# Kernel optimization log

Hardware: AMD Instinct MI355X
Metric: run time of the kernel (lower is better)

The kernel has to match this reference:

```python
import jax, jax.numpy as jnp
import numpy as np


def setup_inputs() -> dict:
    B, I, H = 4096, 512, 1024
    key = jax.random.key(0)
    ks = jax.random.split(key, 10)
    return {
        "input": jax.random.normal(ks[0], (B, I), dtype=jnp.float32),
        "t": jax.random.uniform(ks[1], (B, 1), dtype=jnp.float32),
        "hx": jax.random.normal(ks[2], (B, H), dtype=jnp.float32),
        "cx": jax.random.normal(ks[3], (B, H), dtype=jnp.float32),
        "weight_ih": jax.random.normal(ks[4], (4 * H, I), dtype=jnp.float32),
        "weight_hh": jax.random.normal(ks[5], (4 * H, H), dtype=jnp.float32),
        "bias_ih": jax.random.normal(ks[6], (4 * H,), dtype=jnp.float32),
        "bias_hh": jax.random.normal(ks[7], (4 * H,), dtype=jnp.float32),
        "W_decomp": jax.random.normal(ks[8], (H, H), dtype=jnp.float32),
        "b_decomp": jax.random.normal(ks[9], (H,), dtype=jnp.float32),
    }


def reference(input, t, hx, cx, weight_ih, weight_hh, bias_ih, bias_hh, W_decomp, b_decomp):
    H = W_decomp.shape[0]
    # gates: [B, 4H]
    gates = input @ weight_ih.T + bias_ih + hx @ weight_hh.T + bias_hh
    ingate, forgetgate, cellgate, outgate = jnp.split(gates, 4, axis=1)
    # time-decay factor g(t): elementwise 1/t where t != 0, broadcast [B,1] -> [B,H]
    T = jnp.where(t != 0, 1.0 / jnp.where(t != 0, t, 1.0), 0.0)  # [B, 1]
    T = jnp.broadcast_to(T, (t.shape[0], H))
    # T-LSTM cell-state decomposition
    C_ST = jnp.tanh(cx @ W_decomp + b_decomp)
    cx_adj = cx - C_ST + T * C_ST
    ingate = jax.nn.sigmoid(ingate)
    forgetgate = jax.nn.sigmoid(forgetgate)
    cellgate = jnp.tanh(cellgate)
    outgate = jax.nn.sigmoid(outgate)
    cy = forgetgate * cx_adj + ingate * cellgate
    hy = outgate * jnp.tanh(cy)
    return (hy, cy)
```

## Files before the change

kernel.cpp:

```cpp
#include <hip/hip_runtime.h>
#include <cstdint>


typedef __attribute__((ext_vector_type(8))) __bf16 bf16x8;
typedef __attribute__((ext_vector_type(4))) float f32x4;

__device__ __forceinline__ unsigned short f2bf_rn(float f) {
  unsigned int u = __float_as_uint(f);
  unsigned int r = u + 0x7fffu + ((u >> 16) & 1u);
  return (unsigned short)(r >> 16);
}
__device__ __forceinline__ float bf2f(unsigned short h) {
  return __uint_as_float(((unsigned int)h) << 16);
}
__device__ __forceinline__ float sigm_f(float x) {
  return 1.0f / (1.0f + __expf(-x));
}
__device__ __forceinline__ float tanh_f(float x) {
  return 1.0f - 2.0f / (__expf(2.0f * x) + 1.0f);
}
__device__ __forceinline__ void gl_lds16(const void* g, void* l) {
  __builtin_amdgcn_global_load_lds(
      (const __attribute__((address_space(1))) void*)g,
      (__attribute__((address_space(3))) void*)l, 16, 0, 0);
}

__global__ __launch_bounds__(384) void prep_k(
    const float* __restrict__ input, const float* __restrict__ hx,
    const float* __restrict__ w_ih, const float* __restrict__ w_hh,
    const float* __restrict__ cx,
    unsigned short* __restrict__ Xhi, unsigned short* __restrict__ Xlo,
    unsigned short* __restrict__ Whi, unsigned short* __restrict__ Wlo,
    unsigned short* __restrict__ Chi, unsigned short* __restrict__ Clo) {
  const int bid = blockIdx.x;
  const int k = threadIdx.x << 2;
  const float* src;
  unsigned short *hi, *lo;
  if (bid < 4096) {
    const long m = bid;
    src = (k < 512) ? (input + m * 512 + k) : (hx + m * 1024 + (k - 512));
    hi = Xhi + m * 1536 + k;
    lo = Xlo + m * 1536 + k;
  } else if (bid < 8192) {
    const int n = bid - 4096;
    const int g = n >> 10;
    const int h = n & 1023;
    const long nd = ((h >> 5) << 7) | (g << 5) | (h & 31);
    src = (k < 512) ? (w_ih + (long)n * 512 + k) : (w_hh + (long)n * 1024 + (k - 512));
    hi = Whi + nd * 1536 + k;
    lo = Wlo + nd * 1536 + k;
  } else {
    if (k >= 1024) return;
    const long m = bid - 8192;
    src = cx + m * 1024 + k;
    hi = Chi + m * 1024 + k;
    lo = Clo + m * 1024 + k;
  }
  float4 v = *(const float4*)src;
  ushort4 hv, lv;
  hv.x = f2bf_rn(v.x); lv.x = f2bf_rn(v.x - bf2f(hv.x));
  hv.y = f2bf_rn(v.y); lv.y = f2bf_rn(v.y - bf2f(hv.y));
  hv.z = f2bf_rn(v.z); lv.z = f2bf_rn(v.z - bf2f(hv.z));
  hv.w = f2bf_rn(v.w); lv.w = f2bf_rn(v.w - bf2f(hv.w));
  *(ushort4*)hi = hv;
  *(ushort4*)lo = lv;
}

__global__ void transpose_split_k(const float* __restrict__ W, int Ndim,
                                  unsigned short* __restrict__ Thi,
                                  unsigned short* __restrict__ Tlo) {
  __shared__ float tile[64][65];
  const int bx = blockIdx.x * 64;
  const int by = blockIdx.y * 64;
  const int tx = threadIdx.x;
  for (int r = threadIdx.y; r < 64; r += 4)
    tile[r][tx] = W[(long)(by + r) * Ndim + bx + tx];
  __syncthreads();
  for (int r = threadIdx.y; r < 64; r += 4) {
    float v = tile[tx][r];
    unsigned short h = f2bf_rn(v);
    long o = (long)(bx + r) * Ndim + by + tx;
    Thi[o] = h;
    Tlo[o] = f2bf_rn(v - bf2f(h));
  }
}

__global__ __launch_bounds__(256) void gemm_mega(
    const unsigned short* __restrict__ Xh, const unsigned short* __restrict__ Xl,
    const unsigned short* __restrict__ Wh, const unsigned short* __restrict__ Wl,
    const unsigned short* __restrict__ Ch, const unsigned short* __restrict__ Cl,
    const unsigned short* __restrict__ Dh, const unsigned short* __restrict__ Dl,
    const float* __restrict__ b_ih, const float* __restrict__ b_hh,
    const float* __restrict__ b_d, const float* __restrict__ cx,
    const float* __restrict__ t, float* __restrict__ out) {
  __shared__ __align__(16) unsigned short sAh[128 * 32];
  __shared__ __align__(16) unsigned short sAl[128 * 32];
  __shared__ __align__(16) unsigned short sBh[128 * 32];
  __shared__ __align__(16) unsigned short sBl[128 * 32];

  const int n_blk = blockIdx.x & 31;
  const int m_blk = blockIdx.x >> 5;
  const int m0 = m_blk * 128;
  const int n0 = n_blk * 128;
  const int h0 = n_blk * 32;

  const int tid = threadIdx.x;
  const int wave = tid >> 6;
  const int lane = tid & 63;
  const int srow = lane >> 2;
  const int ssw = (((lane & 3) ^ ((lane >> 3) & 3)) << 3);
  const int fm = lane & 15;
  const int fq = lane >> 4;
  const int psw = (fq ^ ((fm >> 1) & 3)) << 3;

  f32x4 dacc[2][2];
#pragma unroll
  for (int i = 0; i < 2; ++i)
#pragma unroll
    for (int j = 0; j < 2; ++j) dacc[i][j] = {0.f, 0.f, 0.f, 0.f};

  {
    const unsigned short* dsrc = (wave < 2) ? Dh : Dl;
    unsigned short* ddst = ((wave < 2) ? sBh : sBl) + ((wave & 1) * 16) * 32;
    const long dgbase = (long)(h0 + (wave & 1) * 16 + srow) * 1024 + ssw;
    for (int kt = 0; kt < 1024; kt += 32) {
#pragma unroll
      for (int r = 0; r < 2; ++r) {
        const int rowb = r * 64 + wave * 16;
        const long gA = (long)(m0 + rowb + srow) * 1024 + kt + ssw;
        gl_lds16(Ch + gA, sAh + rowb * 32);
        gl_lds16(Cl + gA, sAl + rowb * 32);
      }
      gl_lds16(dsrc + dgbase + kt, ddst);
      __syncthreads();
      bf16x8 ah[2], al[2], bh[2], bl[2];
#pragma unroll
      for (int i = 0; i < 2; ++i) {
        const int ao = (wave * 32 + i * 16 + fm) * 32 + psw;
        ah[i] = *(const bf16x8*)(sAh + ao);
        al[i] = *(const bf16x8*)(sAl + ao);
        const int bo = (i * 16 + fm) * 32 + psw;
        bh[i] = *(const bf16x8*)(sBh + bo);
        bl[i] = *(const bf16x8*)(sBl + bo);
      }
#pragma unroll
      for (int i = 0; i < 2; ++i)
#pragma unroll
        for (int j = 0; j < 2; ++j) {
          dacc[i][j] = __builtin_amdgcn_mfma_f32_16x16x32_bf16(ah[i], bh[j], dacc[i][j], 0, 0, 0);
          dacc[i][j] = __builtin_amdgcn_mfma_f32_16x16x32_bf16(ah[i], bl[j], dacc[i][j], 0, 0, 0);
          dacc[i][j] = __builtin_amdgcn_mfma_f32_16x16x32_bf16(al[i], bh[j], dacc[i][j], 0, 0, 0);
        }
      __syncthreads();
    }
  }

  f32x4 acc[2][8];
#pragma unroll
  for (int i = 0; i < 2; ++i)
#pragma unroll
    for (int j = 0; j < 8; ++j) acc[i][j] = {0.f, 0.f, 0.f, 0.f};

  for (int kt = 0; kt < 1536; kt += 32) {
#pragma unroll
    for (int r = 0; r < 2; ++r) {
      const int rowb = r * 64 + wave * 16;
      const long gA = (long)(m0 + rowb + srow) * 1536 + kt + ssw;
      const long gB = (long)(n0 + rowb + srow) * 1536 + kt + ssw;
      gl_lds16(Xh + gA, sAh + rowb * 32);
      gl_lds16(Xl + gA, sAl + rowb * 32);
      gl_lds16(Wh + gB, sBh + rowb * 32);
      gl_lds16(Wl + gB, sBl + rowb * 32);
    }
    __syncthreads();
    bf16x8 ah[2], al[2];
#pragma unroll
    for (int i = 0; i < 2; ++i) {
      const int ao = (wave * 32 + i * 16 + fm) * 32 + psw;
      ah[i] = *(const bf16x8*)(sAh + ao);
      al[i] = *(const bf16x8*)(sAl + ao);
    }
#pragma unroll
    for (int jh = 0; jh < 2; ++jh) {
      bf16x8 bh[4], bl[4];
#pragma unroll
      for (int jj = 0; jj < 4; ++jj) {
        const int bo = ((jh * 4 + jj) * 16 + fm) * 32 + psw;
        bh[jj] = *(const bf16x8*)(sBh + bo);
        bl[jj] = *(const bf16x8*)(sBl + bo);
      }
#pragma unroll
      for (int i = 0; i < 2; ++i)
#pragma unroll
        for (int jj = 0; jj < 4; ++jj) {
          const int j = jh * 4 + jj;
          acc[i][j] = __builtin_amdgcn_mfma_f32_16x16x32_bf16(ah[i], bh[jj], acc[i][j], 0, 0, 0);
          acc[i][j] = __builtin_amdgcn_mfma_f32_16x16x32_bf16(ah[i], bl[jj], acc[i][j], 0, 0, 0);
          acc[i][j] = __builtin_amdgcn_mfma_f32_16x16x32_bf16(al[i], bh[jj], acc[i][j], 0, 0, 0);
        }
    }
    __syncthreads();
  }

#pragma unroll
  for (int j0 = 0; j0 < 2; ++j0) {
    const int h = h0 + j0 * 16 + fm;
    const float bsum_i = b_ih[h]           + b_hh[h];
    const float bsum_f = b_ih[1024 + h]    + b_hh[1024 + h];
    const float bsum_g = b_ih[2048 + h]    + b_hh[2048 + h];
    const float bsum_o = b_ih[3072 + h]    + b_hh[3072 + h];
    const float bd = b_d[h];
#pragma unroll
    for (int i = 0; i < 2; ++i) {
#pragma unroll
      for (int r = 0; r < 4; ++r) {
        const int m = m0 + wave * 32 + i * 16 + fq * 4 + r;
        const float tv = t[m];
        const float T = (tv != 0.0f) ? (1.0f / tv) : 0.0f;
        const float cst = tanh_f(dacc[i][j0][r] + bd);
        const float cadj = cx[(long)m * 1024 + h] + (T - 1.0f) * cst;
        const float ig = sigm_f(acc[i][0 + j0][r] + bsum_i);
        const float fg = sigm_f(acc[i][2 + j0][r] + bsum_f);
        const float cg = tanh_f(acc[i][4 + j0][r] + bsum_g);
        const float og = sigm_f(acc[i][6 + j0][r] + bsum_o);
        const float cy = fg * cadj + ig * cg;
        const float hy = og * tanh_f(cy);
        out[(long)m * 1024 + h] = hy;
        out[4096L * 1024 + (long)m * 1024 + h] = cy;
      }
    }
  }
}

extern "C" void kernel_launch(void* const* d_in, const int* in_sizes, int n_in,
                              void* d_out, int out_size, void* d_ws, size_t ws_size,
                              hipStream_t stream) {
  const float* input = (const float*)d_in[0];
  const float* t     = (const float*)d_in[1];
  const float* hx    = (const float*)d_in[2];
  const float* cx    = (const float*)d_in[3];
  const float* w_ih  = (const float*)d_in[4];
  const float* w_hh  = (const float*)d_in[5];
  const float* b_ih  = (const float*)d_in[6];
  const float* b_hh  = (const float*)d_in[7];
  const float* Wd    = (const float*)d_in[8];
  const float* b_d   = (const float*)d_in[9];

  const long B = 4096, H = 1024, KX = 1536, NG = 4096;

  char* ws = (char*)d_ws;
  unsigned short* Xhi = (unsigned short*)ws; ws += B * KX * 2;
  unsigned short* Xlo = (unsigned short*)ws; ws += B * KX * 2;
  unsigned short* Whi = (unsigned short*)ws; ws += NG * KX * 2;
  unsigned short* Wlo = (unsigned short*)ws; ws += NG * KX * 2;
  unsigned short* Chi = (unsigned short*)ws; ws += B * H * 2;
  unsigned short* Clo = (unsigned short*)ws; ws += B * H * 2;
  unsigned short* Dhi = (unsigned short*)ws; ws += H * H * 2;
  unsigned short* Dlo = (unsigned short*)ws; ws += H * H * 2;

  prep_k<<<12288, 384, 0, stream>>>(input, hx, w_ih, w_hh, cx,
                                    Xhi, Xlo, Whi, Wlo, Chi, Clo);
  transpose_split_k<<<dim3(16, 16), dim3(64, 4), 0, stream>>>(Wd, 1024, Dhi, Dlo);
  gemm_mega<<<1024, 256, 0, stream>>>(Xhi, Xlo, Whi, Wlo, Chi, Clo, Dhi, Dlo,
                                      b_ih, b_hh, b_d, cx, t, (float*)d_out);
}
```

Measured before the change: 329.9 us.

## Double-buffer LDS, enlarge M tile to 256 with 8 waves, swizzle block order

Makes the fused GEMM use a 256x128 block tile computed by 8 waves in a 4x2 grid. LDS buffers are double-buffered, so the global-to-LDS loads for the next k-step are issued before computing the current one, with explicit vmcnt waits and raw barriers. The gate-weight interleave changes to 16-column groups to match the new per-wave N split, and blocks are swizzled for L2 locality. MFMA sections are wrapped in raised wave priority. The intent is to hide load latency and raise reuse, at the cost of more LDS and registers, which may limit occupancy.

After: 360.0 us. +9.1%, slower.

```diff
diff --git a/kernel.cpp b/kernel.cpp
--- a/kernel.cpp
+++ b/kernel.cpp
@@ -45,7 +45,7 @@
     const int n = bid - 4096;
     const int g = n >> 10;
     const int h = n & 1023;
-    const long nd = ((h >> 5) << 7) | (g << 5) | (h & 31);
+    const long nd = ((long)(h >> 4) << 6) | (g << 4) | (h & 15);
     src = (k < 512) ? (w_ih + (long)n * 512 + k) : (w_hh + (long)n * 1024 + (k - 512));
     hi = Whi + nd * 1536 + k;
     lo = Wlo + nd * 1536 + k;
@@ -85,7 +85,7 @@
   }
 }
 
-__global__ __launch_bounds__(256) void gemm_mega(
+__global__ __launch_bounds__(512, 2) void gemm_mega(
     const unsigned short* __restrict__ Xh, const unsigned short* __restrict__ Xl,
     const unsigned short* __restrict__ Wh, const unsigned short* __restrict__ Wl,
     const unsigned short* __restrict__ Ch, const unsigned short* __restrict__ Cl,
@@ -93,143 +93,165 @@
     const float* __restrict__ b_ih, const float* __restrict__ b_hh,
     const float* __restrict__ b_d, const float* __restrict__ cx,
     const float* __restrict__ t, float* __restrict__ out) {
-  __shared__ __align__(16) unsigned short sAh[128 * 32];
-  __shared__ __align__(16) unsigned short sAl[128 * 32];
-  __shared__ __align__(16) unsigned short sBh[128 * 32];
-  __shared__ __align__(16) unsigned short sBl[128 * 32];
-
-  const int n_blk = blockIdx.x & 31;
-  const int m_blk = blockIdx.x >> 5;
-  const int m0 = m_blk * 128;
+  __shared__ __align__(16) unsigned short sAh[2][8192];
+  __shared__ __align__(16) unsigned short sAl[2][8192];
+  __shared__ __align__(16) unsigned short sBh[2][4096];
+  __shared__ __align__(16) unsigned short sBl[2][4096];
+
+  const int swz = ((blockIdx.x & 7) << 6) | (blockIdx.x >> 3);
+  const int n_blk = swz & 31;
+  const int m_blk = swz >> 5;
+  const int m0 = m_blk * 256;
   const int n0 = n_blk * 128;
   const int h0 = n_blk * 32;
 
   const int tid = threadIdx.x;
   const int wave = tid >> 6;
   const int lane = tid & 63;
+  const int wr = wave >> 1;
+  const int wc = wave & 1;
   const int srow = lane >> 2;
   const int ssw = (((lane & 3) ^ ((lane >> 3) & 3)) << 3);
   const int fm = lane & 15;
   const int fq = lane >> 4;
   const int psw = (fq ^ ((fm >> 1) & 3)) << 3;
 
-  f32x4 dacc[2][2];
-#pragma unroll
-  for (int i = 0; i < 2; ++i)
-#pragma unroll
-    for (int j = 0; j < 2; ++j) dacc[i][j] = {0.f, 0.f, 0.f, 0.f};
-
-  {
-    const unsigned short* dsrc = (wave < 2) ? Dh : Dl;
-    unsigned short* ddst = ((wave < 2) ? sBh : sBl) + ((wave & 1) * 16) * 32;
-    const long dgbase = (long)(h0 + (wave & 1) * 16 + srow) * 1024 + ssw;
-    for (int kt = 0; kt < 1024; kt += 32) {
-#pragma unroll
-      for (int r = 0; r < 2; ++r) {
-        const int rowb = r * 64 + wave * 16;
-        const long gA = (long)(m0 + rowb + srow) * 1024 + kt + ssw;
-        gl_lds16(Ch + gA, sAh + rowb * 32);
-        gl_lds16(Cl + gA, sAl + rowb * 32);
+#define STAGE1(B_, KT_)                                                        \
+  {                                                                            \
+    const long gA0 = (long)(m0 + wave * 32 + srow) * 1024 + (KT_) + ssw;       \
+    gl_lds16(Ch + gA0, &sAh[B_][(wave * 32) * 32]);                            \
+    gl_lds16(Cl + gA0, &sAl[B_][(wave * 32) * 32]);                            \
+    const long gA1 = gA0 + 16 * 1024;                                          \
+    gl_lds16(Ch + gA1, &sAh[B_][(wave * 32 + 16) * 32]);                       \
+    gl_lds16(Cl + gA1, &sAl[B_][(wave * 32 + 16) * 32]);                       \
+    if (wave < 4) {                                                            \
+      const int rb = (wave & 1) * 16;                                          \
+      const long gD = (long)(h0 + rb + srow) * 1024 + (KT_) + ssw;             \
+      if (wave & 2) gl_lds16(Dl + gD, &sBl[B_][rb * 32]);                      \
+      else          gl_lds16(Dh + gD, &sBh[B_][rb * 32]);                      \
+    }                                                                          \
+  }
+
+#define STAGE2(B_, KT_)                                                        \
+  {                                                                            \
+    const long gA0 = (long)(m0 + wave * 32 + srow) * 1536 + (KT_) + ssw;       \
+    gl_lds16(Xh + gA0, &sAh[B_][(wave * 32) * 32]);                            \
+    gl_lds16(Xl + gA0, &sAl[B_][(wave * 32) * 32]);                            \
+    const long gA1 = gA0 + 16 * 1536;                                          \
+    gl_lds16(Xh + gA1, &sAh[B_][(wave * 32 + 16) * 32]);                       \
+    gl_lds16(Xl + gA1, &sAl[B_][(wave * 32 + 16) * 32]);                       \
+    const long gB0 = (long)(n0 + wave * 16 + srow) * 1536 + (KT_) + ssw;       \
+    gl_lds16(Wh + gB0, &sBh[B_][(wave * 16) * 32]);                            \
+    gl_lds16(Wl + gB0, &sBl[B_][(wave * 16) * 32]);                            \
+  }
+
+  f32x4 dacc[4];
+#pragma unroll
+  for (int i = 0; i < 4; ++i) dacc[i] = {0.f, 0.f, 0.f, 0.f};
+
+  STAGE1(0, 0);
+#pragma unroll 2
+  for (int it = 0; it < 32; ++it) {
+    const int b = it & 1;
+    if (it < 31) {
+      STAGE1(b ^ 1, (it + 1) * 32);
+      if (wave < 4) asm volatile("s_waitcnt vmcnt(5)" ::: "memory");
+      else          asm volatile("s_waitcnt vmcnt(4)" ::: "memory");
+    } else {
+      asm volatile("s_waitcnt vmcnt(0)" ::: "memory");
+    }
+    __builtin_amdgcn_s_barrier();
+    bf16x8 ah[4], al[4];
+#pragma unroll
+    for (int mf = 0; mf < 4; ++mf) {
+      const int ao = (wr * 64 + mf * 16 + fm) * 32 + psw;
+      ah[mf] = *(const bf16x8*)&sAh[b][ao];
+      al[mf] = *(const bf16x8*)&sAl[b][ao];
+    }
+    const int bo = (wc * 16 + fm) * 32 + psw;
+    const bf16x8 bh = *(const bf16x8*)&sBh[b][bo];
+    const bf16x8 bl = *(const bf16x8*)&sBl[b][bo];
+    __builtin_amdgcn_s_setprio(1);
+#pragma unroll
+    for (int mf = 0; mf < 4; ++mf) {
+      dacc[mf] = __builtin_amdgcn_mfma_f32_16x16x32_bf16(ah[mf], bh, dacc[mf], 0, 0, 0);
+      dacc[mf] = __builtin_amdgcn_mfma_f32_16x16x32_bf16(ah[mf], bl, dacc[mf], 0, 0, 0);
+      dacc[mf] = __builtin_amdgcn_mfma_f32_16x16x32_bf16(al[mf], bh, dacc[mf], 0, 0, 0);
+    }
+    __builtin_amdgcn_s_setprio(0);
+    __builtin_amdgcn_s_barrier();
+  }
+
+  f32x4 acc[4][4];
+#pragma unroll
+  for (int i = 0; i < 4; ++i)
+#pragma unroll
+    for (int j = 0; j < 4; ++j) acc[i][j] = {0.f, 0.f, 0.f, 0.f};
+
+  STAGE2(0, 0);
+#pragma unroll 2
+  for (int it = 0; it < 48; ++it) {
+    const int b = it & 1;
+    if (it < 47) {
+      STAGE2(b ^ 1, (it + 1) * 32);
+      asm volatile("s_waitcnt vmcnt(6)" ::: "memory");
+    } else {
+      asm volatile("s_waitcnt vmcnt(0)" ::: "memory");
+    }
+    __builtin_amdgcn_s_barrier();
+    bf16x8 ah[4], al[4], bh[4], bl[4];
+#pragma unroll
+    for (int mf = 0; mf < 4; ++mf) {
+      const int ao = (wr * 64 + mf * 16 + fm) * 32 + psw;
+      ah[mf] = *(const bf16x8*)&sAh[b][ao];
+      al[mf] = *(const bf16x8*)&sAl[b][ao];
+    }
+#pragma unroll
+    for (int nf = 0; nf < 4; ++nf) {
+      const int bo = (wc * 64 + nf * 16 + fm) * 32 + psw;
+      bh[nf] = *(const bf16x8*)&sBh[b][bo];
+      bl[nf] = *(const bf16x8*)&sBl[b][bo];
+    }
+    __builtin_amdgcn_s_setprio(1);
+#pragma unroll
+    for (int nf = 0; nf < 4; ++nf)
+#pragma unroll
+      for (int mf = 0; mf < 4; ++mf) {
+        acc[mf][nf] = __builtin_amdgcn_mfma_f32_16x16x32_bf16(ah[mf], bh[nf], acc[mf][nf], 0, 0, 0);
+        acc[mf][nf] = __builtin_amdgcn_mfma_f32_16x16x32_bf16(ah[mf], bl[nf], acc[mf][nf], 0, 0, 0);
+        acc[mf][nf] = __builtin_amdgcn_mfma_f32_16x16x32_bf16(al[mf], bh[nf], acc[mf][nf], 0, 0, 0);
       }
-      gl_lds16(dsrc + dgbase + kt, ddst);
-      __syncthreads();
-      bf16x8 ah[2], al[2], bh[2], bl[2];
-#pragma unroll
-      for (int i = 0; i < 2; ++i) {
-        const int ao = (wave * 32 + i * 16 + fm) * 32 + psw;
-        ah[i] = *(const bf16x8*)(sAh + ao);
-        al[i] = *(const bf16x8*)(sAl + ao);
-        const int bo = (i * 16 + fm) * 32 + psw;
-        bh[i] = *(const bf16x8*)(sBh + bo);
-        bl[i] = *(const bf16x8*)(sBl + bo);
-      }
-#pragma unroll
-      for (int i = 0; i < 2; ++i)
-#pragma unroll
-        for (int j = 0; j < 2; ++j) {
-          dacc[i][j] = __builtin_amdgcn_mfma_f32_16x16x32_bf16(ah[i], bh[j], dacc[i][j], 0, 0, 0);
-          dacc[i][j] = __builtin_amdgcn_mfma_f32_16x16x32_bf16(ah[i], bl[j], dacc[i][j], 0, 0, 0);
-          dacc[i][j] = __builtin_amdgcn_mfma_f32_16x16x32_bf16(al[i], bh[j], dacc[i][j], 0, 0, 0);
-        }
-      __syncthreads();
-    }
-  }
-
-  f32x4 acc[2][8];
-#pragma unroll
-  for (int i = 0; i < 2; ++i)
-#pragma unroll
-    for (int j = 0; j < 8; ++j) acc[i][j] = {0.f, 0.f, 0.f, 0.f};
-
-  for (int kt = 0; kt < 1536; kt += 32) {
-#pragma unroll
-    for (int r = 0; r < 2; ++r) {
-      const int rowb = r * 64 + wave * 16;
-      const long gA = (long)(m0 + rowb + srow) * 1536 + kt + ssw;
-      const long gB = (long)(n0 + rowb + srow) * 1536 + kt + ssw;
-      gl_lds16(Xh + gA, sAh + rowb * 32);
-      gl_lds16(Xl + gA, sAl + rowb * 32);
-      gl_lds16(Wh + gB, sBh + rowb * 32);
-      gl_lds16(Wl + gB, sBl + rowb * 32);
-    }
-    __syncthreads();
-    bf16x8 ah[2], al[2];
-#pragma unroll
-    for (int i = 0; i < 2; ++i) {
-      const int ao = (wave * 32 + i * 16 + fm) * 32 + psw;
-      ah[i] = *(const bf16x8*)(sAh + ao);
-      al[i] = *(const bf16x8*)(sAl + ao);
-    }
-#pragma unroll
-    for (int jh = 0; jh < 2; ++jh) {
-      bf16x8 bh[4], bl[4];
-#pragma unroll
-      for (int jj = 0; jj < 4; ++jj) {
-        const int bo = ((jh * 4 + jj) * 16 + fm) * 32 + psw;
-        bh[jj] = *(const bf16x8*)(sBh + bo);
-        bl[jj] = *(const bf16x8*)(sBl + bo);
-      }
-#pragma unroll
-      for (int i = 0; i < 2; ++i)
-#pragma unroll
-        for (int jj = 0; jj < 4; ++jj) {
-          const int j = jh * 4 + jj;
-          acc[i][j] = __builtin_amdgcn_mfma_f32_16x16x32_bf16(ah[i], bh[jj], acc[i][j], 0, 0, 0);
-          acc[i][j] = __builtin_amdgcn_mfma_f32_16x16x32_bf16(ah[i], bl[jj], acc[i][j], 0, 0, 0);
-          acc[i][j] = __builtin_amdgcn_mfma_f32_16x16x32_bf16(al[i], bh[jj], acc[i][j], 0, 0, 0);
-        }
-    }
-    __syncthreads();
-  }
-
-#pragma unroll
-  for (int j0 = 0; j0 < 2; ++j0) {
-    const int h = h0 + j0 * 16 + fm;
-    const float bsum_i = b_ih[h]           + b_hh[h];
-    const float bsum_f = b_ih[1024 + h]    + b_hh[1024 + h];
-    const float bsum_g = b_ih[2048 + h]    + b_hh[2048 + h];
-    const float bsum_o = b_ih[3072 + h]    + b_hh[3072 + h];
-    const float bd = b_d[h];
-#pragma unroll
-    for (int i = 0; i < 2; ++i) {
-#pragma unroll
-      for (int r = 0; r < 4; ++r) {
-        const int m = m0 + wave * 32 + i * 16 + fq * 4 + r;
-        const float tv = t[m];
-        const float T = (tv != 0.0f) ? (1.0f / tv) : 0.0f;
-        const float cst = tanh_f(dacc[i][j0][r] + bd);
-        const float cadj = cx[(long)m * 1024 + h] + (T - 1.0f) * cst;
-        const float ig = sigm_f(acc[i][0 + j0][r] + bsum_i);
-        const float fg = sigm_f(acc[i][2 + j0][r] + bsum_f);
-        const float cg = tanh_f(acc[i][4 + j0][r] + bsum_g);
-        const float og = sigm_f(acc[i][6 + j0][r] + bsum_o);
-        const float cy = fg * cadj + ig * cg;
-        const float hy = og * tanh_f(cy);
-        out[(long)m * 1024 + h] = hy;
-        out[4096L * 1024 + (long)m * 1024 + h] = cy;
-      }
-    }
-  }
+    __builtin_amdgcn_s_setprio(0);
+    __builtin_amdgcn_s_barrier();
+  }
+
+  const int h = h0 + wc * 16 + fm;
+  const float bi  = b_ih[h]        + b_hh[h];
+  const float bff = b_ih[1024 + h] + b_hh[1024 + h];
+  const float bg  = b_ih[2048 + h] + b_hh[2048 + h];
+  const float bo2 = b_ih[3072 + h] + b_hh[3072 + h];
+  const float bd  = b_d[h];
+#pragma unroll
+  for (int mf = 0; mf < 4; ++mf) {
+#pragma unroll
+    for (int r = 0; r < 4; ++r) {
+      const int m = m0 + wr * 64 + mf * 16 + fq * 4 + r;
+      const float tv = t[m];
+      const float T = (tv != 0.0f) ? (1.0f / tv) : 0.0f;
+      const float cst = tanh_f(dacc[mf][r] + bd);
+      const float cadj = cx[(long)m * 1024 + h] + (T - 1.0f) * cst;
+      const float ig = sigm_f(acc[mf][0][r] + bi);
+      const float fg = sigm_f(acc[mf][1][r] + bff);
+      const float cg = tanh_f(acc[mf][2][r] + bg);
+      const float og = sigm_f(acc[mf][3][r] + bo2);
+      const float cyv = fg * cadj + ig * cg;
+      const float hyv = og * tanh_f(cyv);
+      out[(long)m * 1024 + h] = hyv;
+      out[4096L * 1024 + (long)m * 1024 + h] = cyv;
+    }
+  }
+#undef STAGE1
+#undef STAGE2
 }
 
 extern "C" void kernel_launch(void* const* d_in, const int* in_sizes, int n_in,
@@ -261,6 +283,6 @@
   prep_k<<<12288, 384, 0, stream>>>(input, hx, w_ih, w_hh, cx,
                                     Xhi, Xlo, Whi, Wlo, Chi, Clo);
   transpose_split_k<<<dim3(16, 16), dim3(64, 4), 0, stream>>>(Wd, 1024, Dhi, Dlo);
-  gemm_mega<<<1024, 256, 0, stream>>>(Xhi, Xlo, Whi, Wlo, Chi, Clo, Dhi, Dlo,
-                                      b_ih, b_hh, b_d, cx, t, (float*)d_out);
-}
+  gemm_mega<<<512, 512, 0, stream>>>(Xhi, Xlo, Whi, Wlo, Chi, Clo, Dhi, Dlo,
+                                     b_ih, b_hh, b_d, cx, t, (float*)d_out);
+}
```
